# Kernel tuning notes

Measured on AMD Instinct MI355X. Metric: run time of the kernel, lower is better.

Reference implementation:

```python
import jax, jax.numpy as jnp
import numpy as np

KAPPA = 5.0
EPS_NORM = 1e-12  # torch F.normalize eps
EPS_LOG = 1e-09


def setup_inputs() -> dict:
    key = jax.random.key(0)
    student_output = jax.random.normal(key, (16384, 256), dtype=jnp.float32)
    return {"student_output": student_output}


def reference(student_output) -> jnp.ndarray:
    # L2-normalize rows (matches F.normalize: x / max(||x||, eps))
    norm = jnp.linalg.norm(student_output, axis=-1, keepdims=True)
    x_norm = student_output / jnp.maximum(norm, EPS_NORM)
    # pairwise cosine similarity [n, n]
    sim = x_norm @ x_norm.T
    kernel = jnp.exp(KAPPA * sim)
    density_estimates = kernel.sum(axis=1)  # [n]
    entropy = -jnp.mean(jnp.log(density_estimates + EPS_LOG))
    return entropy
```

## Files before the change

kernel.cpp:

```cpp
#include <hip/hip_runtime.h>


#define NROWS 16384
#define KDIM 256
#define NTILE 128
#define NT (NROWS / NTILE)
#define NSTRIP 4
#define TOTAL_BLOCKS (NT * NSTRIP)

#define SQRT_KLOG2E 2.68579577857f

typedef int i32x4_t __attribute__((ext_vector_type(4)));
typedef int i32x8_t __attribute__((ext_vector_type(8)));
typedef float f32x2_t __attribute__((ext_vector_type(2)));
typedef float f32x16_t __attribute__((ext_vector_type(16)));
typedef __attribute__((address_space(1))) const void global_cvoid_t;
typedef __attribute__((address_space(3))) void lds_void_t;

#if __has_builtin(__builtin_amdgcn_exp2f)
#define EXP2(x) __builtin_amdgcn_exp2f(x)
#else
#define EXP2(x) exp2f(x)
#endif

union frag8 { i32x8_t v8; i32x4_t v4[2]; };

__global__ __launch_bounds__(256)
void kde_normalize(const float* __restrict__ X, unsigned int* __restrict__ Xn8,
                   float* __restrict__ density, unsigned int* __restrict__ ticket) {
  const int wave = threadIdx.x >> 6;
  const int lane = threadIdx.x & 63;
  const int row = blockIdx.x * 4 + wave;
  const float4 v = ((const float4*)(X + (size_t)row * KDIM))[lane];
  float ss = v.x * v.x + v.y * v.y + v.z * v.z + v.w * v.w;
  ss += __shfl_xor(ss, 1);
  ss += __shfl_xor(ss, 2);
  ss += __shfl_xor(ss, 4);
  ss += __shfl_xor(ss, 8);
  ss += __shfl_xor(ss, 16);
  ss += __shfl_xor(ss, 32);
  const float scale = SQRT_KLOG2E / fmaxf(sqrtf(ss), 1e-12f);
  int p = 0;
  p = __builtin_amdgcn_cvt_pk_fp8_f32(v.x * scale, v.y * scale, p, false);
  p = __builtin_amdgcn_cvt_pk_fp8_f32(v.z * scale, v.w * scale, p, true);
  Xn8[(size_t)row * 64 + lane] = (unsigned int)p;
  if (threadIdx.x < 4) density[blockIdx.x * 4 + threadIdx.x] = 0.0f;
  if (blockIdx.x == 0 && threadIdx.x == 0) *ticket = 0u;
}

__global__ __launch_bounds__(256, 2)
void kde_gemm(const unsigned char* __restrict__ Xn8, float* __restrict__ density,
              unsigned int* __restrict__ ticket, float* __restrict__ out) {
  extern __shared__ char smem[];
  char* buf0 = smem;
  char* buf1 = smem + 32768;

  const int tid = threadIdx.x;
  const int wave = tid >> 6;
  const int lane = tid & 63;
  const int wr2 = wave >> 1;
  const int wc2 = wave & 1;
  const int m32 = lane & 31;
  const int h = lane >> 5;
  const int bi = blockIdx.x;
  const int s = blockIdx.y;
  const int t0 = s * 16;
  const int nt = (s == 0 && bi < NT / 2) ? 17 : 16;
  const char* Xb = (const char*)Xn8;

#define STAGE(base_row, dst)                                                      \
  for (int c = wave; c < 32; c += 4) {                                            \
    const int rt = c >> 3, kb = (c >> 1) & 3, hh = c & 1;                         \
    const size_t gofs =                                                           \
        (size_t)((base_row) + rt * 32 + m32) * KDIM + kb * 64 + h * 32 + hh * 16; \
    __builtin_amdgcn_global_load_lds((global_cvoid_t*)(Xb + gofs),                \
                                     (lds_void_t*)((dst) + c * 1024), 16, 0, 0);  \
  }

  STAGE(bi * NTILE, buf0);
  STAGE(((bi + t0) & (NT - 1)) * NTILE, buf1);
  __syncthreads();

  frag8 areg[2][4];
#pragma unroll
  for (int rt = 0; rt < 2; rt++)
#pragma unroll
    for (int kb = 0; kb < 4; kb++) {
      const char* pa =
          buf0 + (((wr2 * 2 + rt) * 8) + kb * 2) * 1024 + lane * 16;
      areg[rt][kb].v4[0] = *(const i32x4_t*)pa;
      areg[rt][kb].v4[1] = *(const i32x4_t*)(pa + 1024);
    }
  __syncthreads();

  f32x2_t rs2[2][8];
#pragma unroll
  for (int rt = 0; rt < 2; rt++)
#pragma unroll
    for (int r = 0; r < 8; r++) rs2[rt][r] = (f32x2_t)0.0f;

  for (int k = 0; k < nt; ++k) {
    const int t = (k == 16) ? 64 : (t0 + k);
    const int J = (bi + t) & (NT - 1);
    char* rbuf = (k & 1) ? buf0 : buf1;
    char* sbuf = (k & 1) ? buf1 : buf0;

    if (k + 1 < nt) {
      const int tn = (k + 1 == 16) ? 64 : (t0 + k + 1);
      STAGE(((bi + tn) & (NT - 1)) * NTILE, sbuf);
    }

    f32x16_t acc[2][2];
#pragma unroll
    for (int rt = 0; rt < 2; rt++)
#pragma unroll
      for (int ct = 0; ct < 2; ct++) acc[rt][ct] = (f32x16_t)0.0f;

#pragma unroll
    for (int kb = 0; kb < 4; ++kb) {
      frag8 bf[2];
#pragma unroll
      for (int ct = 0; ct < 2; ct++) {
        const char* pb =
            rbuf + (((wc2 * 2 + ct) * 8) + kb * 2) * 1024 + lane * 16;
        bf[ct].v4[0] = *(const i32x4_t*)pb;
        bf[ct].v4[1] = *(const i32x4_t*)(pb + 1024);
      }
#pragma unroll
      for (int rt = 0; rt < 2; rt++)
#pragma unroll
        for (int ct = 0; ct < 2; ct++)
          acc[rt][ct] = __builtin_amdgcn_mfma_scale_f32_32x32x64_f8f6f4(
              areg[rt][kb].v8, bf[ct].v8, acc[rt][ct], 0, 0, 0, 127, 0, 127);
    }

#pragma unroll
    for (int ct = 0; ct < 2; ct++) {
      f32x2_t c2 = (f32x2_t)0.0f;
#pragma unroll
      for (int rt = 0; rt < 2; rt++)
#pragma unroll
        for (int r2 = 0; r2 < 8; r2++) {
          f32x2_t e;
          e.x = EXP2(acc[rt][ct][2 * r2]);
          e.y = EXP2(acc[rt][ct][2 * r2 + 1]);
          rs2[rt][r2] += e;
          c2 += e;
        }
      if (t != 0) {
        float cs = c2.x + c2.y;
        cs += __shfl_xor(cs, 32);
        if (h == 0)
          atomicAdd(&density[J * NTILE + wc2 * 64 + ct * 32 + m32], cs);
      }
    }

    __syncthreads();
  }

#pragma unroll
  for (int rt = 0; rt < 2; rt++)
#pragma unroll
    for (int r = 0; r < 16; r++) {
      float v = rs2[rt][r >> 1][r & 1];
      v += __shfl_xor(v, 1);
      v += __shfl_xor(v, 2);
      v += __shfl_xor(v, 4);
      v += __shfl_xor(v, 8);
      v += __shfl_xor(v, 16);
      if (m32 == 0) {
        const int row = bi * NTILE + wr2 * 64 + rt * 32 +
                        (r & 3) + 8 * (r >> 2) + 4 * h;
        atomicAdd(&density[row], v);
      }
    }
#undef STAGE

  __syncthreads();
  if (tid == 0) {
    __threadfence();
    ((volatile unsigned int*)smem)[0] = atomicAdd(ticket, 1u);
  }
  __syncthreads();
  if (((volatile unsigned int*)smem)[0] == TOTAL_BLOCKS - 1) {
    __threadfence();
    float ssum = 0.0f;
    for (int i = tid; i < NROWS; i += 256) {
      const float d = __hip_atomic_load(&density[i], __ATOMIC_RELAXED,
                                        __HIP_MEMORY_SCOPE_AGENT);
      ssum += logf(d + 1e-9f);
    }
    ssum += __shfl_xor(ssum, 1);
    ssum += __shfl_xor(ssum, 2);
    ssum += __shfl_xor(ssum, 4);
    ssum += __shfl_xor(ssum, 8);
    ssum += __shfl_xor(ssum, 16);
    ssum += __shfl_xor(ssum, 32);
    float* red = ((float*)smem) + 16;
    if (lane == 0) red[wave] = ssum;
    __syncthreads();
    if (tid == 0) {
      float tot = 0.0f;
      for (int w = 0; w < 4; w++) tot += red[w];
      out[0] = -tot / (float)NROWS;
    }
  }
}

extern "C" void kernel_launch(void* const* d_in, const int* in_sizes, int n_in,
                              void* d_out, int out_size, void* d_ws, size_t ws_size,
                              hipStream_t stream) {
  const float* X = (const float*)d_in[0];
  float* out = (float*)d_out;
  char* ws = (char*)d_ws;
  unsigned int* Xn8 = (unsigned int*)ws;
  float* density = (float*)(ws + (size_t)NROWS * KDIM);
  unsigned int* ticket = (unsigned int*)(density + NROWS);

  hipFuncSetAttribute((const void*)kde_gemm,
                      hipFuncAttributeMaxDynamicSharedMemorySize, 65536);

  kde_normalize<<<NROWS / 4, 256, 0, stream>>>(X, Xn8, density, ticket);
  kde_gemm<<<dim3(NT, NSTRIP), 256, 65536, stream>>>((const unsigned char*)ws,
                                                     density, ticket, out);
}
```

Baseline: 136.6 us.

## Drop LDS staging: pre-swizzle fp8 into MFMA fragment layout, load B straight to registers

The normalize kernel now writes fp8 data in a fragment-ordered layout, so each 16-byte lane load maps directly onto the MFMA operand. The GEMM kernel drops shared-memory staging and barriers and streams B fragments from global/L2 into two register buffers, software-pipelined one column tile ahead. Blocks shrink to two waves, each owning 64 rows, and the strip count doubles to keep the grid large. This removes LDS traffic and syncs, but every wave now re-reads B tiles from cache instead of sharing them through LDS, which raises L2 bandwidth pressure.

Result: slower. 221.9 us (+62.5%).

```diff
diff --git a/kernel.cpp b/kernel.cpp
--- a/kernel.cpp
+++ b/kernel.cpp
@@ -5,7 +5,7 @@
 #define KDIM 256
 #define NTILE 128
 #define NT (NROWS / NTILE)
-#define NSTRIP 4
+#define NSTRIP 8
 #define TOTAL_BLOCKS (NT * NSTRIP)
 
 #define SQRT_KLOG2E 2.68579577857f
@@ -14,8 +14,6 @@
 typedef int i32x8_t __attribute__((ext_vector_type(8)));
 typedef float f32x2_t __attribute__((ext_vector_type(2)));
 typedef float f32x16_t __attribute__((ext_vector_type(16)));
-typedef __attribute__((address_space(1))) const void global_cvoid_t;
-typedef __attribute__((address_space(3))) void lds_void_t;
 
 #if __has_builtin(__builtin_amdgcn_exp2f)
 #define EXP2(x) __builtin_amdgcn_exp2f(x)
@@ -25,8 +23,9 @@
 
 union frag8 { i32x8_t v8; i32x4_t v4[2]; };
 
+
 __global__ __launch_bounds__(256)
-void kde_normalize(const float* __restrict__ X, unsigned int* __restrict__ Xn8,
+void kde_normalize(const float* __restrict__ X, unsigned char* __restrict__ XnF,
                    float* __restrict__ density, unsigned int* __restrict__ ticket) {
   const int wave = threadIdx.x >> 6;
   const int lane = threadIdx.x & 63;
@@ -43,55 +42,44 @@
   int p = 0;
   p = __builtin_amdgcn_cvt_pk_fp8_f32(v.x * scale, v.y * scale, p, false);
   p = __builtin_amdgcn_cvt_pk_fp8_f32(v.z * scale, v.w * scale, p, true);
-  Xn8[(size_t)row * 64 + lane] = (unsigned int)p;
+  const int piece = lane >> 2;
+  const size_t addr = (size_t)(row >> 5) * 8192 +
+                      (((piece >> 2) * 2 + (piece & 1)) * 1024) +
+                      (((piece >> 1) & 1) * 512) + ((row & 31) * 16) +
+                      ((lane & 3) * 4);
+  *(unsigned int*)(XnF + addr) = (unsigned int)p;
   if (threadIdx.x < 4) density[blockIdx.x * 4 + threadIdx.x] = 0.0f;
   if (blockIdx.x == 0 && threadIdx.x == 0) *ticket = 0u;
 }
 
-__global__ __launch_bounds__(256, 2)
+__global__ __launch_bounds__(128, 2)
 void kde_gemm(const unsigned char* __restrict__ Xn8, float* __restrict__ density,
               unsigned int* __restrict__ ticket, float* __restrict__ out) {
-  extern __shared__ char smem[];
-  char* buf0 = smem;
-  char* buf1 = smem + 32768;
+  __shared__ float red[2];
+  __shared__ unsigned int tick_s;
 
   const int tid = threadIdx.x;
   const int wave = tid >> 6;
   const int lane = tid & 63;
-  const int wr2 = wave >> 1;
-  const int wc2 = wave & 1;
   const int m32 = lane & 31;
   const int h = lane >> 5;
   const int bi = blockIdx.x;
   const int s = blockIdx.y;
-  const int t0 = s * 16;
-  const int nt = (s == 0 && bi < NT / 2) ? 17 : 16;
+  const int t0 = s * 8;
+  const int nt = (s == 0 && bi < NT / 2) ? 9 : 8;
   const char* Xb = (const char*)Xn8;
-
-#define STAGE(base_row, dst)                                                      \
-  for (int c = wave; c < 32; c += 4) {                                            \
-    const int rt = c >> 3, kb = (c >> 1) & 3, hh = c & 1;                         \
-    const size_t gofs =                                                           \
-        (size_t)((base_row) + rt * 32 + m32) * KDIM + kb * 64 + h * 32 + hh * 16; \
-    __builtin_amdgcn_global_load_lds((global_cvoid_t*)(Xb + gofs),                \
-                                     (lds_void_t*)((dst) + c * 1024), 16, 0, 0);  \
-  }
-
-  STAGE(bi * NTILE, buf0);
-  STAGE(((bi + t0) & (NT - 1)) * NTILE, buf1);
-  __syncthreads();
+  const int lofs = lane * 16;
 
   frag8 areg[2][4];
 #pragma unroll
   for (int rt = 0; rt < 2; rt++)
 #pragma unroll
-    for (int kb = 0; kb < 4; kb++) {
-      const char* pa =
-          buf0 + (((wr2 * 2 + rt) * 8) + kb * 2) * 1024 + lane * 16;
-      areg[rt][kb].v4[0] = *(const i32x4_t*)pa;
-      areg[rt][kb].v4[1] = *(const i32x4_t*)(pa + 1024);
-    }
-  __syncthreads();
+    for (int kb = 0; kb < 4; kb++)
+#pragma unroll
+      for (int pp = 0; pp < 2; pp++)
+        areg[rt][kb].v4[pp] = *(const i32x4_t*)(
+            Xb + (size_t)(bi * 4 + wave * 2 + rt) * 8192 +
+            (kb * 2 + pp) * 1024 + lofs);
 
   f32x2_t rs2[2][8];
 #pragma unroll
@@ -99,64 +87,72 @@
 #pragma unroll
     for (int r = 0; r < 8; r++) rs2[rt][r] = (f32x2_t)0.0f;
 
+  frag8 bA[4], bB[4];
+
+#define LOADB(BUF, J, CT)                                                   \
+  {                                                                         \
+    const char* pb_ = Xb + (size_t)((J) * 4 + (CT)) * 8192 + lofs;          \
+    _Pragma("unroll")                                                       \
+    for (int kb = 0; kb < 4; kb++) {                                        \
+      BUF[kb].v4[0] = *(const i32x4_t*)(pb_ + (kb * 2) * 1024);             \
+      BUF[kb].v4[1] = *(const i32x4_t*)(pb_ + (kb * 2 + 1) * 1024);         \
+    }                                                                       \
+  }
+
+#define EPIRT(ACCV, RT)                                                     \
+  {                                                                         \
+    _Pragma("unroll")                                                       \
+    for (int r2 = 0; r2 < 8; r2++) {                                        \
+      f32x2_t e;                                                            \
+      e.x = EXP2(ACCV[2 * r2]);                                             \
+      e.y = EXP2(ACCV[2 * r2 + 1]);                                         \
+      rs2[RT][r2] += e;                                   \
+      cacc += e;                                                            \
+    }                                                                       \
+  }
+
+#define CTSTEP(BUFC, BUFN, CT, PRE, JNEXT, CTN)                             \
+  {                                                                         \
+    if (PRE) LOADB(BUFN, JNEXT, CTN);                                       \
+    f32x16_t a0 = __builtin_amdgcn_mfma_scale_f32_32x32x64_f8f6f4(          \
+        areg[0][0].v8, BUFC[0].v8, (f32x16_t)0.0f, 0, 0, 0, 127, 0, 127);   \
+    f32x16_t a1 = __builtin_amdgcn_mfma_scale_f32_32x32x64_f8f6f4(          \
+        areg[1][0].v8, BUFC[0].v8, (f32x16_t)0.0f, 0, 0, 0, 127, 0, 127);   \
+    _Pragma("unroll")                                                       \
+    for (int kb = 1; kb < 4; kb++) {                                        \
+      a0 = __builtin_amdgcn_mfma_scale_f32_32x32x64_f8f6f4(                 \
+          areg[0][kb].v8, BUFC[kb].v8, a0, 0, 0, 0, 127, 0, 127);           \
+      a1 = __builtin_amdgcn_mfma_scale_f32_32x32x64_f8f6f4(                 \
+          areg[1][kb].v8, BUFC[kb].v8, a1, 0, 0, 0, 127, 0, 127);           \
+    }                                                                       \
+    f32x2_t cacc = (f32x2_t)0.0f;                                           \
+    EPIRT(a0, 0)                                                            \
+    EPIRT(a1, 1)                                                            \
+    if (t != 0) {                           \
+      float cs_ = cacc.x + cacc.y;                                          \
+      cs_ += __shfl_xor(cs_, 32);    \
+      if (h == 0) atomicAdd(&density[Jc * NTILE + (CT) * 32 + m32], cs_);   \
+    }                                                                       \
+  }
+
+  int Jc = (bi + t0) & (NT - 1);
+  LOADB(bA, Jc, 0);
+
   for (int k = 0; k < nt; ++k) {
-    const int t = (k == 16) ? 64 : (t0 + k);
-    const int J = (bi + t) & (NT - 1);
-    char* rbuf = (k & 1) ? buf0 : buf1;
-    char* sbuf = (k & 1) ? buf1 : buf0;
-
-    if (k + 1 < nt) {
-      const int tn = (k + 1 == 16) ? 64 : (t0 + k + 1);
-      STAGE(((bi + tn) & (NT - 1)) * NTILE, sbuf);
-    }
-
-    f32x16_t acc[2][2];
-#pragma unroll
-    for (int rt = 0; rt < 2; rt++)
-#pragma unroll
-      for (int ct = 0; ct < 2; ct++) acc[rt][ct] = (f32x16_t)0.0f;
-
-#pragma unroll
-    for (int kb = 0; kb < 4; ++kb) {
-      frag8 bf[2];
-#pragma unroll
-      for (int ct = 0; ct < 2; ct++) {
-        const char* pb =
-            rbuf + (((wc2 * 2 + ct) * 8) + kb * 2) * 1024 + lane * 16;
-        bf[ct].v4[0] = *(const i32x4_t*)pb;
-        bf[ct].v4[1] = *(const i32x4_t*)(pb + 1024);
-      }
-#pragma unroll
-      for (int rt = 0; rt < 2; rt++)
-#pragma unroll
-        for (int ct = 0; ct < 2; ct++)
-          acc[rt][ct] = __builtin_amdgcn_mfma_scale_f32_32x32x64_f8f6f4(
-              areg[rt][kb].v8, bf[ct].v8, acc[rt][ct], 0, 0, 0, 127, 0, 127);
-    }
-
-#pragma unroll
-    for (int ct = 0; ct < 2; ct++) {
-      f32x2_t c2 = (f32x2_t)0.0f;
-#pragma unroll
-      for (int rt = 0; rt < 2; rt++)
-#pragma unroll
-        for (int r2 = 0; r2 < 8; r2++) {
-          f32x2_t e;
-          e.x = EXP2(acc[rt][ct][2 * r2]);
-          e.y = EXP2(acc[rt][ct][2 * r2 + 1]);
-          rs2[rt][r2] += e;
-          c2 += e;
-        }
-      if (t != 0) {
-        float cs = c2.x + c2.y;
-        cs += __shfl_xor(cs, 32);
-        if (h == 0)
-          atomicAdd(&density[J * NTILE + wc2 * 64 + ct * 32 + m32], cs);
-      }
-    }
-
-    __syncthreads();
-  }
+    const int t = (k == 8) ? 64 : (t0 + k);
+    Jc = (bi + t) & (NT - 1);
+    const bool pre = (k + 1 < nt);
+    const int tn = (k + 1 == 8) ? 64 : (t0 + k + 1);
+    const int Jn = (bi + tn) & (NT - 1);
+
+    CTSTEP(bA, bB, 0, true, Jc, 1);
+    CTSTEP(bB, bA, 1, true, Jc, 2);
+    CTSTEP(bA, bB, 2, true, Jc, 3);
+    CTSTEP(bB, bA, 3, pre, Jn, 0);
+  }
+#undef LOADB
+#undef EPIRT
+#undef CTSTEP
 
 #pragma unroll
   for (int rt = 0; rt < 2; rt++)
@@ -169,23 +165,22 @@
       v += __shfl_xor(v, 8);
       v += __shfl_xor(v, 16);
       if (m32 == 0) {
-        const int row = bi * NTILE + wr2 * 64 + rt * 32 +
+        const int row = bi * NTILE + wave * 64 + rt * 32 +
                         (r & 3) + 8 * (r >> 2) + 4 * h;
         atomicAdd(&density[row], v);
       }
     }
-#undef STAGE
 
   __syncthreads();
   if (tid == 0) {
     __threadfence();
-    ((volatile unsigned int*)smem)[0] = atomicAdd(ticket, 1u);
+    tick_s = atomicAdd(ticket, 1u);
   }
   __syncthreads();
-  if (((volatile unsigned int*)smem)[0] == TOTAL_BLOCKS - 1) {
+  if (tick_s == TOTAL_BLOCKS - 1) {
     __threadfence();
     float ssum = 0.0f;
-    for (int i = tid; i < NROWS; i += 256) {
+    for (int i = tid; i < NROWS; i += 128) {
       const float d = __hip_atomic_load(&density[i], __ATOMIC_RELAXED,
                                         __HIP_MEMORY_SCOPE_AGENT);
       ssum += logf(d + 1e-9f);
@@ -196,14 +191,9 @@
     ssum += __shfl_xor(ssum, 8);
     ssum += __shfl_xor(ssum, 16);
     ssum += __shfl_xor(ssum, 32);
-    float* red = ((float*)smem) + 16;
     if (lane == 0) red[wave] = ssum;
     __syncthreads();
-    if (tid == 0) {
-      float tot = 0.0f;
-      for (int w = 0; w < 4; w++) tot += red[w];
-      out[0] = -tot / (float)NROWS;
-    }
+    if (tid == 0) out[0] = -(red[0] + red[1]) / (float)NROWS;
   }
 }
 
@@ -213,14 +203,10 @@
   const float* X = (const float*)d_in[0];
   float* out = (float*)d_out;
   char* ws = (char*)d_ws;
-  unsigned int* Xn8 = (unsigned int*)ws;
+  unsigned char* XnF = (unsigned char*)ws;
   float* density = (float*)(ws + (size_t)NROWS * KDIM);
   unsigned int* ticket = (unsigned int*)(density + NROWS);
 
-  hipFuncSetAttribute((const void*)kde_gemm,
-                      hipFuncAttributeMaxDynamicSharedMemorySize, 65536);
-
-  kde_normalize<<<NROWS / 4, 256, 0, stream>>>(X, Xn8, density, ticket);
-  kde_gemm<<<dim3(NT, NSTRIP), 256, 65536, stream>>>((const unsigned char*)ws,
-                                                     density, ticket, out);
+  kde_normalize<<<NROWS / 4, 256, 0, stream>>>(X, XnF, density, ticket);
+  kde_gemm<<<dim3(NT, NSTRIP), 128, 0, stream>>>(XnF, density, ticket, out);
 }
```
